# Performance work log

Hardware: AMD Instinct MI355X
Metric: run time of the kernel (lower is better)

## Reference

```python
import jax, jax.numpy as jnp
import numpy as np

N_NODES = 100000
D_IN = 256
D_OUT = 128
N_EDGES = 1600000


def setup_inputs() -> dict:
    key = jax.random.key(0)
    k1, k2, k3, k4 = jax.random.split(key, 4)
    x = jax.random.normal(k1, (N_NODES, D_IN), dtype=jnp.float32)
    edge_index = jax.random.randint(k2, (2, N_EDGES), 0, N_NODES, dtype=jnp.int64)
    # GCNConv parameters (glorot-style scale)
    W = jax.random.normal(k3, (D_IN, D_OUT), dtype=jnp.float32) * (1.0 / np.sqrt(D_IN))
    b = jax.random.normal(k4, (D_OUT,), dtype=jnp.float32) * 0.01
    return {"x": x, "edge_index": edge_index, "W": W, "b": b}


def reference(x, edge_index, W, b):
    n = x.shape[0]
    # add self-loops (PyG GCNConv default)
    loop = jnp.arange(n, dtype=edge_index.dtype)
    src = jnp.concatenate([edge_index[0], loop])
    dst = jnp.concatenate([edge_index[1], loop])
    # symmetric normalization: deg^-1/2[src] * deg^-1/2[dst]
    ones = jnp.ones(src.shape[0], dtype=x.dtype)
    deg = jax.ops.segment_sum(ones, dst, num_segments=n)
    dinv = jnp.where(deg > 0, jax.lax.rsqrt(deg), 0.0)
    norm = dinv[src] * dinv[dst]  # [E+N]
    # linear transform at nodes, then gather-scale-scatter over edges
    h = x @ W  # [N, d_out]
    msg = h[src] * norm[:, None]  # [E+N, d_out]
    out = jax.ops.segment_sum(msg, dst, num_segments=n) + b
    # CRD.forward: relu then dropout (identity in eval mode)
    return jax.nn.relu(out)
```

## Files before the change

kernel.cpp:

```cpp
#include <hip/hip_runtime.h>
#include <stdint.h>

#define D_IN 256
#define D_OUT 128
#define BUCKET_CAP 64

typedef __attribute__((ext_vector_type(8))) short bf16x8;
typedef __attribute__((ext_vector_type(4))) float f32x4;

__device__ __forceinline__ unsigned short f2bf(float f) {
  union { float f; uint32_t u; } v; v.f = f;
  uint32_t u = v.u;
  uint32_t r = (u + 0x7FFFu + ((u >> 16) & 1u)) >> 16;
  return (unsigned short)r;
}

__device__ __forceinline__ float bfbits2f(uint32_t bits) {
  union { uint32_t u; float f; } v; v.u = bits;
  return v.f;
}

__global__ __launch_bounds__(256) void k_zero(int* __restrict__ p, int n) {
  int i = blockIdx.x * 256 + threadIdx.x;
  if (i < n) p[i] = 0;
}

__global__ __launch_bounds__(256) void k_conv_w(const float* __restrict__ W,
                                                unsigned short* __restrict__ wt) {
  int idx = blockIdx.x * 256 + threadIdx.x;
  int n = idx >> 8;
  int k = idx & 255;
  wt[idx] = f2bf(W[k * D_OUT + n]);
}

__global__ __launch_bounds__(256) void k_fused(const float* __restrict__ x,
                                               const unsigned short* __restrict__ wt,
                                               unsigned short* __restrict__ hp,
                                               int N,
                                               const int* __restrict__ ei, int E,
                                               int* __restrict__ cnt,
                                               int* __restrict__ bkt,
                                               int Gg, int R) {
  int k = blockIdx.x;
  bool is_gemm = ((k % R) == 0) && ((k / R) < Gg);
  if (is_gemm) {
    int gid = k / R;
    int wave = threadIdx.x >> 6;
    int lane = threadIdx.x & 63;
    int m = lane & 15;
    int q = lane >> 4;
    int r0 = gid * 64 + wave * 16;
    if (r0 >= N) return;

    bf16x8 a[8];
    const float* xrow = x + (size_t)(r0 + m) * D_IN + q * 8;
#pragma unroll
    for (int kt = 0; kt < 8; ++kt) {
      float4 u0 = *reinterpret_cast<const float4*>(xrow + kt * 32);
      float4 u1 = *reinterpret_cast<const float4*>(xrow + kt * 32 + 4);
      bf16x8 av;
      av[0] = (short)f2bf(u0.x); av[1] = (short)f2bf(u0.y);
      av[2] = (short)f2bf(u0.z); av[3] = (short)f2bf(u0.w);
      av[4] = (short)f2bf(u1.x); av[5] = (short)f2bf(u1.y);
      av[6] = (short)f2bf(u1.z); av[7] = (short)f2bf(u1.w);
      a[kt] = av;
    }

#pragma unroll
    for (int nt = 0; nt < 8; ++nt) {
      f32x4 acc = {0.f, 0.f, 0.f, 0.f};
      const unsigned short* wrow = wt + (size_t)(nt * 16 + m) * D_IN + q * 8;
#pragma unroll
      for (int kt = 0; kt < 8; ++kt) {
        bf16x8 bv = *reinterpret_cast<const bf16x8*>(wrow + kt * 32);
        acc = __builtin_amdgcn_mfma_f32_16x16x32_bf16(a[kt], bv, acc, 0, 0, 0);
      }
#pragma unroll
      for (int r = 0; r < 4; ++r) {
        int row = r0 + q * 4 + r;
        hp[(size_t)row * D_OUT + nt * 16 + m] = f2bf(acc[r]);
      }
    }
  } else {
    int hid = k - min((k + R - 1) / R, Gg);
    int e = hid * 256 + threadIdx.x;
    if (e >= E) return;
    int s = ei[e];
    int d = ei[E + e];
    int pos = atomicAdd(&cnt[d], 1);
    if (pos < BUCKET_CAP) bkt[d * BUCKET_CAP + pos] = s;
  }
}

__global__ __launch_bounds__(256) void k_agg(const unsigned short* __restrict__ hp,
                                             const int* __restrict__ bkt,
                                             const int* __restrict__ cnt,
                                             const float* __restrict__ bias,
                                             float* __restrict__ out, int N) {
  __shared__ int s_src[4][BUCKET_CAP];
  int wave = threadIdx.x >> 6;
  int lane = threadIdx.x & 63;
  int node = blockIdx.x * 4 + wave;
  int c_true = cnt[node];
  int c = c_true < BUCKET_CAP ? c_true : BUCKET_CAP;
  if (lane < c) s_src[wave][lane] = bkt[node * BUCKET_CAP + lane];
  __syncthreads();

  float rs_self = rsqrtf(1.0f + (float)c_true);
  const uint32_t* hrow_self =
      reinterpret_cast<const uint32_t*>(hp + (size_t)node * D_OUT) + lane;
  uint32_t us = *hrow_self;
  float acc0 = rs_self * bfbits2f(us << 16);
  float acc1 = rs_self * bfbits2f(us & 0xFFFF0000u);

  int e = 0;
  for (; e + 4 <= c; e += 4) {
    int s0 = s_src[wave][e];
    int s1 = s_src[wave][e + 1];
    int s2 = s_src[wave][e + 2];
    int s3 = s_src[wave][e + 3];
    uint32_t u0 = reinterpret_cast<const uint32_t*>(hp + (size_t)s0 * D_OUT)[lane];
    uint32_t u1 = reinterpret_cast<const uint32_t*>(hp + (size_t)s1 * D_OUT)[lane];
    uint32_t u2 = reinterpret_cast<const uint32_t*>(hp + (size_t)s2 * D_OUT)[lane];
    uint32_t u3 = reinterpret_cast<const uint32_t*>(hp + (size_t)s3 * D_OUT)[lane];
    int c0 = cnt[s0], c1 = cnt[s1], c2 = cnt[s2], c3 = cnt[s3];
    float r0 = rsqrtf(1.0f + (float)c0);
    float r1 = rsqrtf(1.0f + (float)c1);
    float r2 = rsqrtf(1.0f + (float)c2);
    float r3 = rsqrtf(1.0f + (float)c3);
    acc0 += r0 * bfbits2f(u0 << 16) + r1 * bfbits2f(u1 << 16) +
            r2 * bfbits2f(u2 << 16) + r3 * bfbits2f(u3 << 16);
    acc1 += r0 * bfbits2f(u0 & 0xFFFF0000u) + r1 * bfbits2f(u1 & 0xFFFF0000u) +
            r2 * bfbits2f(u2 & 0xFFFF0000u) + r3 * bfbits2f(u3 & 0xFFFF0000u);
  }
  for (; e < c; ++e) {
    int s = s_src[wave][e];
    uint32_t u = reinterpret_cast<const uint32_t*>(hp + (size_t)s * D_OUT)[lane];
    float r = rsqrtf(1.0f + (float)cnt[s]);
    acc0 += r * bfbits2f(u << 16);
    acc1 += r * bfbits2f(u & 0xFFFF0000u);
  }

  float2 bv = *reinterpret_cast<const float2*>(bias + 2 * lane);
  float o0 = rs_self * acc0 + bv.x;
  float o1 = rs_self * acc1 + bv.y;
  float2 ov;
  ov.x = o0 > 0.f ? o0 : 0.f;
  ov.y = o1 > 0.f ? o1 : 0.f;
  *reinterpret_cast<float2*>(out + (size_t)node * D_OUT + 2 * lane) = ov;
}

extern "C" void kernel_launch(void* const* d_in, const int* in_sizes, int n_in,
                              void* d_out, int out_size, void* d_ws, size_t ws_size,
                              hipStream_t stream) {
  const float* x = (const float*)d_in[0];
  const int* ei = (const int*)d_in[1];
  const float* W = (const float*)d_in[2];
  const float* bias = (const float*)d_in[3];
  int N = in_sizes[0] / D_IN;
  int E = in_sizes[1] / 2;
  float* out = (float*)d_out;

  char* w = (char*)d_ws;
  size_t off = 0;
  auto alloc = [&](size_t bytes) -> void* {
    void* p = w + off;
    off = (off + bytes + 255) & ~(size_t)255;
    return p;
  };
  int* cnt = (int*)alloc((size_t)N * 4);
  unsigned short* wt = (unsigned short*)alloc((size_t)D_IN * D_OUT * 2);
  unsigned short* hp = (unsigned short*)alloc((size_t)N * D_OUT * 2);
  int* bkt = (int*)alloc((size_t)N * BUCKET_CAP * 4);
  (void)ws_size; (void)n_in; (void)out_size;

  int Gg = (N + 63) / 64;
  int Gh = (E + 255) / 256;
  int grid = Gg + Gh;
  int R = (grid + Gg - 1) / Gg;

  k_zero<<<(N + 255) / 256, 256, 0, stream>>>(cnt, N);
  k_conv_w<<<(D_IN * D_OUT + 255) / 256, 256, 0, stream>>>(W, wt);
  k_fused<<<grid, 256, 0, stream>>>(x, wt, hp, N, ei, E, cnt, bkt, Gg, R);
  k_agg<<<N / 4, 256, 0, stream>>>(hp, bkt, cnt, bias, out, N);
}
```

Before: 357.1 us.

## Partition edge bucketing by XCD-aligned block slices, precompute dinv, unroll gather by 8

Groups fused-kernel blocks into sets of 8 so that each slice (blockIdx&7) handles only destination nodes with d&7 equal to that slice. The intent is to keep the atomics and bucket writes for a given node local to one XCD's L2, assuming round-robin block placement across XCDs. Each edge-chunk is now read 8 times with vectorised int4 loads. It also adds a small kernel that precomputes the per-node dinv, replacing the per-neighbor cnt loads and rsqrt in aggregation, and unrolls the gather loop to 8 loads in flight.

```diff
diff --git a/kernel.cpp b/kernel.cpp
--- a/kernel.cpp
+++ b/kernel.cpp
@@ -15,9 +15,11 @@
   return (unsigned short)r;
 }
 
-__device__ __forceinline__ float bfbits2f(uint32_t bits) {
-  union { uint32_t u; float f; } v; v.u = bits;
-  return v.f;
+__device__ __forceinline__ float bf_lo(uint32_t u) {
+  union { uint32_t u; float f; } v; v.u = u << 16; return v.f;
+}
+__device__ __forceinline__ float bf_hi(uint32_t u) {
+  union { uint32_t u; float f; } v; v.u = u & 0xFFFF0000u; return v.f;
 }
 
 __global__ __launch_bounds__(256) void k_zero(int* __restrict__ p, int n) {
@@ -31,6 +33,12 @@
   int n = idx >> 8;
   int k = idx & 255;
   wt[idx] = f2bf(W[k * D_OUT + n]);
+}
+
+__global__ __launch_bounds__(256) void k_dinv(const int* __restrict__ cnt,
+                                              float* __restrict__ dinv, int N) {
+  int i = blockIdx.x * 256 + threadIdx.x;
+  if (i < N) dinv[i] = rsqrtf(1.0f + (float)cnt[i]);
 }
 
 __global__ __launch_bounds__(256) void k_fused(const float* __restrict__ x,
@@ -40,16 +48,17 @@
                                                const int* __restrict__ ei, int E,
                                                int* __restrict__ cnt,
                                                int* __restrict__ bkt,
-                                               int Gg, int R) {
-  int k = blockIdx.x;
-  bool is_gemm = ((k % R) == 0) && ((k / R) < Gg);
+                                               int Gg8, int Rg, int Gh8, int CH) {
+  int g8 = blockIdx.x >> 3;
+  int sl = blockIdx.x & 7;
+  bool is_gemm = ((g8 % Rg) == 0) && ((g8 / Rg) < Gg8);
   if (is_gemm) {
-    int gid = k / R;
+    int bid = (g8 / Rg) * 8 + sl;
     int wave = threadIdx.x >> 6;
     int lane = threadIdx.x & 63;
     int m = lane & 15;
     int q = lane >> 4;
-    int r0 = gid * 64 + wave * 16;
+    int r0 = bid * 64 + wave * 16;
     if (r0 >= N) return;
 
     bf16x8 a[8];
@@ -82,63 +91,79 @@
       }
     }
   } else {
-    int hid = k - min((k + R - 1) / R, Gg);
-    int e = hid * 256 + threadIdx.x;
-    if (e >= E) return;
-    int s = ei[e];
-    int d = ei[E + e];
-    int pos = atomicAdd(&cnt[d], 1);
-    if (pos < BUCKET_CAP) bkt[d * BUCKET_CAP + pos] = s;
+    int nb = min(g8 / Rg + 1, Gg8);
+    int hg = g8 - nb;
+    if (hg >= Gh8) return;
+    int start = hg * CH;
+    int end = min(E, start + CH);
+    for (int eb = start + (int)threadIdx.x * 4; eb < end; eb += 1024) {
+      int d4[4];
+      int kmax = end - eb; if (kmax > 4) kmax = 4;
+      if (kmax == 4) {
+        int4 v = *reinterpret_cast<const int4*>(ei + E + eb);
+        d4[0] = v.x; d4[1] = v.y; d4[2] = v.z; d4[3] = v.w;
+      } else {
+        for (int k = 0; k < kmax; ++k) d4[k] = ei[E + eb + k];
+      }
+#pragma unroll
+      for (int k = 0; k < 4; ++k) {
+        if (k >= kmax) break;
+        int d = d4[k];
+        if ((d & 7) == sl) {
+          int s = ei[eb + k];
+          int pos = atomicAdd(&cnt[d], 1);
+          if (pos < BUCKET_CAP) bkt[d * BUCKET_CAP + pos] = s;
+        }
+      }
+    }
   }
 }
 
 __global__ __launch_bounds__(256) void k_agg(const unsigned short* __restrict__ hp,
                                              const int* __restrict__ bkt,
                                              const int* __restrict__ cnt,
+                                             const float* __restrict__ dinv,
                                              const float* __restrict__ bias,
                                              float* __restrict__ out, int N) {
   __shared__ int s_src[4][BUCKET_CAP];
   int wave = threadIdx.x >> 6;
   int lane = threadIdx.x & 63;
   int node = blockIdx.x * 4 + wave;
-  int c_true = cnt[node];
-  int c = c_true < BUCKET_CAP ? c_true : BUCKET_CAP;
+  if (node >= N) return;
+  int c = cnt[node];
+  if (c > BUCKET_CAP) c = BUCKET_CAP;
   if (lane < c) s_src[wave][lane] = bkt[node * BUCKET_CAP + lane];
   __syncthreads();
 
-  float rs_self = rsqrtf(1.0f + (float)c_true);
-  const uint32_t* hrow_self =
-      reinterpret_cast<const uint32_t*>(hp + (size_t)node * D_OUT) + lane;
-  uint32_t us = *hrow_self;
-  float acc0 = rs_self * bfbits2f(us << 16);
-  float acc1 = rs_self * bfbits2f(us & 0xFFFF0000u);
+  float rs_self = dinv[node];
+  uint32_t us = reinterpret_cast<const uint32_t*>(hp + (size_t)node * D_OUT)[lane];
+  float acc0 = rs_self * bf_lo(us);
+  float acc1 = rs_self * bf_hi(us);
 
   int e = 0;
-  for (; e + 4 <= c; e += 4) {
-    int s0 = s_src[wave][e];
-    int s1 = s_src[wave][e + 1];
-    int s2 = s_src[wave][e + 2];
-    int s3 = s_src[wave][e + 3];
-    uint32_t u0 = reinterpret_cast<const uint32_t*>(hp + (size_t)s0 * D_OUT)[lane];
-    uint32_t u1 = reinterpret_cast<const uint32_t*>(hp + (size_t)s1 * D_OUT)[lane];
-    uint32_t u2 = reinterpret_cast<const uint32_t*>(hp + (size_t)s2 * D_OUT)[lane];
-    uint32_t u3 = reinterpret_cast<const uint32_t*>(hp + (size_t)s3 * D_OUT)[lane];
-    int c0 = cnt[s0], c1 = cnt[s1], c2 = cnt[s2], c3 = cnt[s3];
-    float r0 = rsqrtf(1.0f + (float)c0);
-    float r1 = rsqrtf(1.0f + (float)c1);
-    float r2 = rsqrtf(1.0f + (float)c2);
-    float r3 = rsqrtf(1.0f + (float)c3);
-    acc0 += r0 * bfbits2f(u0 << 16) + r1 * bfbits2f(u1 << 16) +
-            r2 * bfbits2f(u2 << 16) + r3 * bfbits2f(u3 << 16);
-    acc1 += r0 * bfbits2f(u0 & 0xFFFF0000u) + r1 * bfbits2f(u1 & 0xFFFF0000u) +
-            r2 * bfbits2f(u2 & 0xFFFF0000u) + r3 * bfbits2f(u3 & 0xFFFF0000u);
+  for (; e + 8 <= c; e += 8) {
+    int s[8];
+    uint32_t u[8];
+    float r[8];
+#pragma unroll
+    for (int j = 0; j < 8; ++j) s[j] = s_src[wave][e + j];
+#pragma unroll
+    for (int j = 0; j < 8; ++j)
+      u[j] = reinterpret_cast<const uint32_t*>(hp + (size_t)s[j] * D_OUT)[lane];
+#pragma unroll
+    for (int j = 0; j < 8; ++j) r[j] = dinv[s[j]];
+#pragma unroll
+    for (int j = 0; j < 8; ++j) {
+      acc0 += r[j] * bf_lo(u[j]);
+      acc1 += r[j] * bf_hi(u[j]);
+    }
   }
   for (; e < c; ++e) {
     int s = s_src[wave][e];
     uint32_t u = reinterpret_cast<const uint32_t*>(hp + (size_t)s * D_OUT)[lane];
-    float r = rsqrtf(1.0f + (float)cnt[s]);
-    acc0 += r * bfbits2f(u << 16);
-    acc1 += r * bfbits2f(u & 0xFFFF0000u);
+    float r = dinv[s];
+    acc0 += r * bf_lo(u);
+    acc1 += r * bf_hi(u);
   }
 
   float2 bv = *reinterpret_cast<const float2*>(bias + 2 * lane);
@@ -169,18 +194,22 @@
     return p;
   };
   int* cnt = (int*)alloc((size_t)N * 4);
+  float* dinv = (float*)alloc((size_t)N * 4);
   unsigned short* wt = (unsigned short*)alloc((size_t)D_IN * D_OUT * 2);
   unsigned short* hp = (unsigned short*)alloc((size_t)N * D_OUT * 2);
   int* bkt = (int*)alloc((size_t)N * BUCKET_CAP * 4);
   (void)ws_size; (void)n_in; (void)out_size;
 
   int Gg = (N + 63) / 64;
-  int Gh = (E + 255) / 256;
-  int grid = Gg + Gh;
-  int R = (grid + Gg - 1) / Gg;
+  int Gg8 = (Gg + 7) / 8;
+  const int CH = 2048;
+  int Gh8 = (E + CH - 1) / CH;
+  int T8 = Gg8 + Gh8;
+  int Rg = (T8 + Gg8 - 1) / Gg8;
 
   k_zero<<<(N + 255) / 256, 256, 0, stream>>>(cnt, N);
   k_conv_w<<<(D_IN * D_OUT + 255) / 256, 256, 0, stream>>>(W, wt);
-  k_fused<<<grid, 256, 0, stream>>>(x, wt, hp, N, ei, E, cnt, bkt, Gg, R);
-  k_agg<<<N / 4, 256, 0, stream>>>(hp, bkt, cnt, bias, out, N);
-}
+  k_fused<<<T8 * 8, 256, 0, stream>>>(x, wt, hp, N, ei, E, cnt, bkt, Gg8, Rg, Gh8, CH);
+  k_dinv<<<(N + 255) / 256, 256, 0, stream>>>(cnt, dinv, N);
+  k_agg<<<(N + 3) / 4, 256, 0, stream>>>(hp, bkt, cnt, dinv, bias, out, N);
+}
```

New measurement: 368.2 us. 1.03x slower.
